# Optimization experiments

Hardware: AMD Instinct MI355X
Metric: run time of the kernel (lower is better)

## Reference

```python
import jax, jax.numpy as jnp
import numpy as np

B, T, H = 256, 48, 512   # batch, timesteps, hidden (= size_seq feature dim)
S = H                    # size_seq == hidden feature dim (dim_seq_in = S+1)
K = 4                    # k_wk_ahead


def setup_inputs() -> dict:
    key = jax.random.key(0)
    ks = jax.random.split(key, 20)
    g = lambda k, shp: (jax.random.normal(k, shp, dtype=jnp.float32) * 0.05)
    inp = {
        "hiddens": jax.random.normal(ks[0], (B, T, S), dtype=jnp.float32),
        "allys": jax.random.normal(ks[1], (B, T), dtype=jnp.float32),
        "k_wk_ahead": K,
        # InputAttention params (Linear stored as [in, out])
        "Wh": g(ks[2], (H, S)), "bh": g(ks[3], (S,)),
        "Ws": g(ks[4], (S, S)), "bs": g(ks[5], (S,)),
        "Wo": g(ks[6], (S, 1)), "bo": g(ks[7], (1,)),
        # GRU params (torch layout: [3H, in]/[3H, H], gates ordered r,z,n)
        "W_ih": g(ks[8], (3 * H, S + 1)), "W_hh": g(ks[9], (3 * H, H)),
        "b_ih": g(ks[10], (3 * H,)), "b_hh": g(ks[11], (3 * H,)),
        # out_layer MLP: H->H/2->H/4->H/8->1 with LeakyReLU after each
        "W1": g(ks[12], (H, H // 2)), "b1": g(ks[13], (H // 2,)),
        "W2": g(ks[14], (H // 2, H // 4)), "b2": g(ks[15], (H // 4,)),
        "W3": g(ks[16], (H // 4, H // 8)), "b3": g(ks[17], (H // 8,)),
        "W4": g(ks[18], (H // 8, 1)), "b4": g(ks[19], (1,)),
    }
    return inp


def _gru_step(x, h, W_ih, W_hh, b_ih, b_hh):
    # torch GRU cell: gates ordered (reset, update, new)
    gi = x @ W_ih.T + b_ih          # [B, 3H]
    gh = h @ W_hh.T + b_hh          # [B, 3H]
    ir, iz, inn = jnp.split(gi, 3, axis=-1)
    hr, hz, hn = jnp.split(gh, 3, axis=-1)
    r = jax.nn.sigmoid(ir + hr)
    z = jax.nn.sigmoid(iz + hz)
    n = jnp.tanh(inn + r * hn)
    return (1.0 - z) * n + z * h


def reference(hiddens, allys, k_wk_ahead, Wh, bh, Ws, bs, Wo, bo,
              W_ih, W_hh, b_ih, b_hh, W1, b1, W2, b2, W3, b3, W4, b4):
    Bb, Tt, Ss = hiddens.shape
    # linearSignals(hiddens) is time-step-invariant: precompute once
    ls = hiddens @ Ws + bs                      # [B, T, S]

    def step(d_prev, ally_t):
        lh = d_prev @ Wh + bh                   # [B, S]
        e = jnp.tanh(lh[:, None, :] + ls) @ Wo + bo    # [B, T, 1]
        att = jax.nn.softmax(e, axis=1)[..., 0]        # [B, T]
        c = jnp.einsum('bt,bts->bs', att, hiddens)     # [B, S]
        x = jnp.concatenate([c, ally_t[:, None]], axis=1)   # [B, S+1]
        d = _gru_step(x, d_prev, W_ih, W_hh, b_ih, b_hh)
        return d, c

    d0 = jnp.zeros((Bb, W_hh.shape[1]), dtype=hiddens.dtype)
    d_last, cs = jax.lax.scan(step, d0, jnp.swapaxes(allys, 0, 1))
    c_last = cs[-1]                             # c_vectors[:, -1]

    def mlp(d):
        h = jax.nn.leaky_relu(d @ W1 + b1)
        h = jax.nn.leaky_relu(h @ W2 + b2)
        h = jax.nn.leaky_relu(h @ W3 + b3)
        return jax.nn.leaky_relu(h @ W4 + b4)   # dropout is identity in eval

    outs = []
    last_d = d_last
    for _ in range(k_wk_ahead):
        out = mlp(last_d)                       # [B, 1]
        outs.append(out)
        x = jnp.concatenate([c_last, out], axis=1)
        last_d = _gru_step(x, last_d, W_ih, W_hh, b_ih, b_hh)
    return jnp.stack(outs, axis=1)[..., 0]      # [B, K]
```

## Files before the change

kernel.cpp:

```cpp
#include <hip/hip_runtime.h>
#include <cstdio>

#ifndef __has_builtin
#define __has_builtin(x) 0
#endif

#define NB      256
#define NT      48
#define NS      512
#define KAHEAD  4
#define NTHREADS 1024
#define NBLOCKS  256
#define GSIZE    32

#define RSTRIDE  528
#define XSLOT    524
#define NKS      33

#define WS_D     0
#define WS_X     135168
#define WS_LH    270336
#define WS_BAR   401408
#define WS_WAH   401664
#define WS_WAL   942336
#define WS_WIH   1483008
#define WS_WIL   1888512
#define WS_FLOATS 2294016

#define L_XHI    0
#define L_XLO    34048
#define L_LSB    68096
#define L_GH     117248
#define L_GI     123776
#define L_LH     130304
#define L_WO     132352
#define L_E      134400
#define L_ATT    134656
#define L_CP     134912
#define L_H1P    136960
#define L_H1S    141056
#define L_H2P    142080
#define L_H2S    144128
#define L_H3P    144640
#define LDS_BYTES 145664

#define XROWB    1064

typedef float  f4v __attribute__((ext_vector_type(4)));
typedef short  s4v __attribute__((ext_vector_type(4)));
typedef unsigned short u4v __attribute__((ext_vector_type(4)));

#if __has_builtin(__builtin_amdgcn_mfma_f32_16x16x16bf16_1k)
__device__ __forceinline__ f4v MFMA16(s4v a, s4v b, f4v c) {
    return __builtin_amdgcn_mfma_f32_16x16x16bf16_1k(a, b, c, 0, 0, 0);
}
#else
typedef short s8v __attribute__((ext_vector_type(8)));
__device__ __forceinline__ f4v MFMA16(s4v a, s4v b, f4v c) {
    s8v A = { a[0], a[1], a[2], a[3], 0, 0, 0, 0 };
    s8v B = { b[0], b[1], b[2], b[3], 0, 0, 0, 0 };
    return __builtin_amdgcn_mfma_f32_16x16x32_bf16(A, B, c, 0, 0, 0);
}
#endif

__device__ __forceinline__ float frcp_(float x) {
#if __has_builtin(__builtin_amdgcn_rcpf)
    return __builtin_amdgcn_rcpf(x);
#else
    return 1.0f / x;
#endif
}
__device__ __forceinline__ float ftanh_(float x) {
    float e = __expf(2.0f * x);
    return 1.0f - 2.0f * frcp_(e + 1.0f);
}
__device__ __forceinline__ float fsig_(float x) { return frcp_(1.0f + __expf(-x)); }
__device__ __forceinline__ float lrelu_(float x) { return fmaxf(x, 0.01f * x); }
__device__ __forceinline__ unsigned short rne16_(unsigned u) {
    return (unsigned short)((u + 0x7FFFu + ((u >> 16) & 1u)) >> 16);
}
__device__ __forceinline__ float bf2f_(unsigned short b) {
    return __uint_as_float(((unsigned)b) << 16);
}
__host__ __device__ __forceinline__ void split2_(float v, unsigned short& hi, unsigned short& lo) {
    unsigned u = __float_as_uint(v);
    unsigned short h = (unsigned short)((u + 0x7FFFu + ((u >> 16) & 1u)) >> 16);
    float hf = __uint_as_float(((unsigned)h) << 16);
    float lof = v - hf;
    unsigned ul = __float_as_uint(lof);
    hi = h;
    lo = (unsigned short)((ul + 0x7FFFu + ((ul >> 16) & 1u)) >> 16);
}

__device__ __forceinline__ void cstore1(float* p, float v) {
    asm volatile("global_store_dword %0, %1, off sc1" :: "v"(p), "v"(v) : "memory");
}
__device__ __forceinline__ f4v cload4(const float* p) {
    f4v v;
    asm volatile("global_load_dwordx4 %0, %1, off sc1" : "=v"(v) : "v"(p));
    return v;
}
__device__ __forceinline__ float cload1(const float* p) {
    float v;
    asm volatile("global_load_dword %0, %1, off sc1" : "=v"(v) : "v"(p));
    return v;
}
__device__ __forceinline__ void cwait() {
    asm volatile("s_waitcnt vmcnt(0)" ::: "memory");
    __builtin_amdgcn_sched_barrier(0);
}

__device__ __forceinline__ void gbar(unsigned* bar, unsigned* epoch) {
    asm volatile("s_waitcnt vmcnt(0)" ::: "memory");
    __syncthreads();
    if (threadIdx.x == 0) {
        *epoch += GSIZE;
        __hip_atomic_fetch_add(bar, 1u, __ATOMIC_RELAXED, __HIP_MEMORY_SCOPE_AGENT);
        unsigned target = *epoch;
        int guard = 0;
        while (__hip_atomic_load(bar, __ATOMIC_RELAXED, __HIP_MEMORY_SCOPE_AGENT) < target) {
#if __has_builtin(__builtin_amdgcn_s_sleep)
            __builtin_amdgcn_s_sleep(2);
#endif
            if (++guard > (1 << 22)) break;
        }
    }
    __syncthreads();
}

__device__ __forceinline__ void cvtStore_(char* hiB, char* loB, int idx, f4v v) {
    unsigned row = (unsigned)idx / 528u;
    unsigned col = (unsigned)idx - row * 528u;
    u4v h, l;
    #pragma unroll
    for (int i = 0; i < 4; ++i) {
        unsigned short hh, ll;
        split2_(v[i], hh, ll);
        h[i] = hh; l[i] = ll;
    }
    *(u4v*)(hiB + row * XROWB + col * 2) = h;
    *(u4v*)(loB + row * XROWB + col * 2) = l;
}

__device__ __forceinline__ void stagePanel(const float* __restrict__ gsrc,
                                           char* __restrict__ hiB,
                                           char* __restrict__ loB, int tid) {
    f4v v0 = cload4(gsrc + tid * 4);
    f4v v1 = cload4(gsrc + 4096 + tid * 4);
    f4v v2 = cload4(gsrc + 8192 + tid * 4);
    f4v v3 = cload4(gsrc + 12288 + tid * 4);
    f4v v4 = {0.f, 0.f, 0.f, 0.f};
    if (tid < 128) v4 = cload4(gsrc + 16384 + tid * 4);
    cwait();
    cvtStore_(hiB, loB, tid * 4, v0);
    cvtStore_(hiB, loB, 4096 + tid * 4, v1);
    cvtStore_(hiB, loB, 8192 + tid * 4, v2);
    cvtStore_(hiB, loB, 12288 + tid * 4, v3);
    if (tid < 128) cvtStore_(hiB, loB, 16384 + tid * 4, v4);
}

__device__ __forceinline__ void gemmA(const char* smem, const unsigned short* BH,
        const unsigned short* BL, int cix, int g, int tid, float* ghs,
        float* lhw, const float* bh, const float* bhh, bool doLH) {
    const int w = tid >> 6;
    if (w >= 8) return;
    const int l = tid & 63, mt = w & 1, nt = w >> 1;
    const char* A  = smem + L_XHI + (mt * 16 + (l & 15)) * XROWB + ((l >> 4) << 3);
    const char* Al = A + (L_XLO - L_XHI);
    const int bbase = ((cix * 4 + nt) * NKS) * 256 + (l << 2);
    f4v acc = {0.f, 0.f, 0.f, 0.f};
    #pragma unroll 3
    for (int ks = 0; ks < NKS; ++ks) {
        s4v ah = *(const s4v*)(A + ks * 32);
        s4v al = *(const s4v*)(Al + ks * 32);
        s4v bhv = *(const s4v*)(BH + bbase + ks * 256);
        s4v blv = *(const s4v*)(BL + bbase + ks * 256);
        acc = MFMA16(ah, bhv, acc);
        acc = MFMA16(al, bhv, acc);
        acc = MFMA16(ah, blv, acc);
    }
    const int jgl = cix * 16 + (l & 15);
    const int rowL = mt * 16 + ((l >> 4) << 2);
    if (nt == 0) {
        if (doLH) {
            float b = bh[jgl];
            #pragma unroll
            for (int r = 0; r < 4; ++r)
                cstore1(lhw + (long)(g * 32 + rowL + r) * NS + jgl, acc[r] + b);
        }
    } else {
        float b = bhh[(nt - 1) * 512 + jgl];
        #pragma unroll
        for (int r = 0; r < 4; ++r)
            ghs[(nt - 1) * 544 + (rowL + r) * 17 + (l & 15)] = acc[r] + b;
    }
}

__device__ __forceinline__ void gemmC(const char* smem, const unsigned short* BH,
        const unsigned short* BL, int cix, int tid, float* gis, const float* bih) {
    const int w = tid >> 6;
    if (w >= 6) return;
    const int l = tid & 63, mt = w & 1, nt = w >> 1;
    const char* A  = smem + L_XHI + (mt * 16 + (l & 15)) * XROWB + ((l >> 4) << 3);
    const char* Al = A + (L_XLO - L_XHI);
    const int bbase = ((cix * 3 + nt) * NKS) * 256 + (l << 2);
    f4v acc = {0.f, 0.f, 0.f, 0.f};
    #pragma unroll 3
    for (int ks = 0; ks < NKS; ++ks) {
        s4v ah = *(const s4v*)(A + ks * 32);
        s4v al = *(const s4v*)(Al + ks * 32);
        s4v bhv = *(const s4v*)(BH + bbase + ks * 256);
        s4v blv = *(const s4v*)(BL + bbase + ks * 256);
        acc = MFMA16(ah, bhv, acc);
        acc = MFMA16(al, bhv, acc);
        acc = MFMA16(ah, blv, acc);
    }
    const int jgl = cix * 16 + (l & 15);
    const int rowL = mt * 16 + ((l >> 4) << 2);
    float b = bih[nt * 512 + jgl];
    #pragma unroll
    for (int r = 0; r < 4; ++r)
        gis[nt * 544 + (rowL + r) * 17 + (l & 15)] = acc[r] + b;
}

__global__ void prep_kernel(const float* __restrict__ Whh,
                            const float* __restrict__ Wih,
                            const float* __restrict__ Wh,
                            float* __restrict__ ws) {
    long i = (long)blockIdx.x * blockDim.x + threadIdx.x;
    long stride = (long)gridDim.x * blockDim.x;
    unsigned short* waH = (unsigned short*)(ws + WS_WAH);
    unsigned short* waL = (unsigned short*)(ws + WS_WAL);
    unsigned short* wiH = (unsigned short*)(ws + WS_WIH);
    unsigned short* wiL = (unsigned short*)(ws + WS_WIL);

    for (long p = i; p < 270336; p += stride) {
        int l = (int)(p & 63);
        int t = (int)(p >> 6);
        int ks = t % NKS, u = t / NKS;
        int nt = u & 3, cix = u >> 2;
        int jg = cix * 16 + (l & 15);
        #pragma unroll
        for (int e = 0; e < 4; ++e) {
            int pc = ks * 16 + ((l >> 4) << 2) + e;
            int kq = pc / 132, ko = pc - kq * 132;
            float wv = 0.f;
            if (ko < 128) {
                int k = kq * 128 + ko;
                wv = (nt == 0) ? Wh[(long)k * 512 + jg]
                               : Whh[((long)((nt - 1) * 512 + jg)) * 512 + k];
            }
            unsigned short hh, ll;
            split2_(wv, hh, ll);
            waH[p * 4 + e] = hh; waL[p * 4 + e] = ll;
        }
    }
    for (long p = i; p < 202752; p += stride) {
        int l = (int)(p & 63);
        int t = (int)(p >> 6);
        int ks = t % NKS, u = t / NKS;
        int nt = u % 3, cix = u / 3;
        int jg = cix * 16 + (l & 15);
        #pragma unroll
        for (int e = 0; e < 4; ++e) {
            int pc = ks * 16 + ((l >> 4) << 2) + e;
            int kq = pc / 132, ko = pc - kq * 132;
            float wv = 0.f;
            int k = -1;
            if (ko < 128) k = kq * 128 + ko;
            else if (pc == XSLOT) k = 512;
            if (k >= 0) wv = Wih[((long)(nt * 512 + jg)) * 513 + k];
            unsigned short hh, ll;
            split2_(wv, hh, ll);
            wiH[p * 4 + e] = hh; wiL[p * 4 + e] = ll;
        }
    }
    for (long p = i; p < 270336; p += stride) ws[WS_D + p] = 0.0f;
    if (i < 256) ((unsigned*)(ws + WS_BAR))[i] = 0u;
}

__global__ void __launch_bounds__(NTHREADS, 4) fused_kernel(
        const float* __restrict__ hiddens, const float* __restrict__ allys,
        const float* __restrict__ Ws, const float* __restrict__ bs,
        const float* __restrict__ Wo, const float* __restrict__ bo,
        const float* __restrict__ bh,
        const float* __restrict__ b_ih, const float* __restrict__ b_hh,
        const float* __restrict__ W1, const float* __restrict__ b1,
        const float* __restrict__ W2, const float* __restrict__ b2,
        const float* __restrict__ W3, const float* __restrict__ b3,
        const float* __restrict__ W4, const float* __restrict__ b4,
        float* __restrict__ ws, float* __restrict__ out) {
    const int tid = threadIdx.x;
    const int bid = blockIdx.x;
    const int g = bid >> 5, cix = bid & 31, myb = bid;

    float* dw  = ws + WS_D;
    float* xw  = ws + WS_X;
    float* lhw = ws + WS_LH;
    const unsigned short* waH = (const unsigned short*)(ws + WS_WAH);
    const unsigned short* waL = (const unsigned short*)(ws + WS_WAL);
    const unsigned short* wiH = (const unsigned short*)(ws + WS_WIH);
    const unsigned short* wiL = (const unsigned short*)(ws + WS_WIL);
    unsigned* bar = (unsigned*)(ws + WS_BAR) + (g << 5);
    unsigned epoch = 0;

    extern __shared__ char smem[];
    char*           xhi   = smem + L_XHI;
    char*           xlo   = smem + L_XLO;
    unsigned short* lsb   = (unsigned short*)(smem + L_LSB);
    float*          ghs   = (float*)(smem + L_GH);
    float*          gis   = (float*)(smem + L_GI);
    float*          lh_s  = (float*)(smem + L_LH);
    float*          wo_s  = (float*)(smem + L_WO);
    float*          e_s   = (float*)(smem + L_E);
    float*          att_s = (float*)(smem + L_ATT);
    float*          cp_s  = (float*)(smem + L_CP);
    float*          h1p   = (float*)(smem + L_H1P);
    float*          h1s   = (float*)(smem + L_H1S);
    float*          h2p   = (float*)(smem + L_H2P);
    float*          h2s   = (float*)(smem + L_H2S);
    float*          h3p   = (float*)(smem + L_H3P);

    const int sS = tid & 511, th = tid >> 9;
    const int rowE = tid >> 4, jE = tid & 15;
    const int jgE = cix * 16 + jE;
    const int jmapE = ((jgE >> 7) * 132) + (jgE & 127);
    const float* gPanelD = dw + (long)g * GSIZE * RSTRIDE;
    const float* gPanelX = xw + (long)g * GSIZE * RSTRIDE;

    float hreg[24];

    if (tid < NS) wo_s[tid] = Wo[tid];

    {
        float* scratch = (float*)(smem + L_XHI);
        for (int ch = 0; ch < 2; ++ch) {
            __syncthreads();
            {
                const float* src = hiddens + ((long)myb * NT + ch * 24) * NS;
                int idx = tid * 12;
                const f4v* s4 = (const f4v*)(src + idx);
                f4v* d4 = (f4v*)(scratch + idx);
                d4[0] = s4[0]; d4[1] = s4[1]; d4[2] = s4[2];
            }
            __syncthreads();
            if (th == ch) {
                #pragma unroll
                for (int q = 0; q < 24; ++q) hreg[q] = scratch[q * 512 + sS];
            }
            {
                const int tl = th * 12;
                float acc[12];
                #pragma unroll
                for (int q = 0; q < 12; ++q) acc[q] = 0.0f;
                for (int k = 0; k < NS; k += 4) {
                    float w0 = Ws[(k + 0) * NS + sS];
                    float w1 = Ws[(k + 1) * NS + sS];
                    float w2 = Ws[(k + 2) * NS + sS];
                    float w3 = Ws[(k + 3) * NS + sS];
                    #pragma unroll
                    for (int q = 0; q < 12; ++q) {
                        f4v h4 = *(const f4v*)(scratch + (tl + q) * 512 + k);
                        acc[q] = fmaf(h4.x, w0, fmaf(h4.y, w1, fmaf(h4.z, w2, fmaf(h4.w, w3, acc[q]))));
                    }
                }
                float bsv = bs[sS];
                #pragma unroll
                for (int q = 0; q < 12; ++q)
                    lsb[(ch * 24 + tl + q) * NS + sS] = rne16_(__float_as_uint(acc[q] + bsv));
            }
        }
    }
    __syncthreads();

    const float bo0 = bo[0];

    for (int t = 0; t < NT; ++t) {
        stagePanel(gPanelD, xhi, xlo, tid);
        __syncthreads();
        gemmA(smem, waH, waL, cix, g, tid, ghs, lhw, bh, b_hh, true);
        gbar(bar, &epoch);

        if (tid < 128) {
            f4v v = cload4(lhw + (long)myb * NS + tid * 4);
            cwait();
            *(f4v*)(lh_s + tid * 4) = v;
        }
        if (tid == 0) cstore1(xw + (long)myb * RSTRIDE + XSLOT, allys[myb * NT + t]);
        __syncthreads();
        {
            const int wv = tid >> 6, ln = tid & 63;
            for (int q = 0; q < 3; ++q) {
                const int tt = wv * 3 + q;
                float p = 0.f;
                #pragma unroll
                for (int i2 = 0; i2 < 8; ++i2) {
                    int s = ln + (i2 << 6);
                    p = fmaf(wo_s[s], ftanh_(lh_s[s] + bf2f_(lsb[tt * NS + s])), p);
                }
                #pragma unroll
                for (int off = 32; off >= 1; off >>= 1) p += __shfl_xor(p, off, 64);
                if (ln == 0) e_s[tt] = p + bo0;
            }
        }
        __syncthreads();
        if (tid < 64) {
            float v = (tid < NT) ? e_s[tid] : -1e30f;
            float m = v;
            #pragma unroll
            for (int off = 32; off >= 1; off >>= 1) m = fmaxf(m, __shfl_xor(m, off, 64));
            float ex = (tid < NT) ? __expf(v - m) : 0.0f;
            float ssum = ex;
            #pragma unroll
            for (int off = 32; off >= 1; off >>= 1) ssum += __shfl_xor(ssum, off, 64);
            if (tid < NT) att_s[tid] = ex * frcp_(ssum);
        }
        __syncthreads();
        {
            float p = 0.f;
            #pragma unroll
            for (int q = 0; q < 24; ++q) p = fmaf(att_s[th * 24 + q], hreg[q], p);
            if (th == 0) cp_s[sS] = p;
            __syncthreads();
            if (th == 1)
                cstore1(xw + (long)myb * RSTRIDE + ((sS >> 7) * 132) + (sS & 127), p + cp_s[sS]);
        }
        gbar(bar, &epoch);

        float hp = 0.f;
        if (tid < 512) hp = cload1(dw + (long)(g * 32 + rowE) * RSTRIDE + jmapE);
        stagePanel(gPanelX, xhi, xlo, tid);
        __syncthreads();
        gemmC(smem, wiH, wiL, cix, tid, gis, b_ih);
        __syncthreads();
        cwait();
        if (tid < 512) {
            float gr = gis[rowE * 17 + jE]        + ghs[rowE * 17 + jE];
            float gz = gis[544 + rowE * 17 + jE]  + ghs[544 + rowE * 17 + jE];
            float gni = gis[1088 + rowE * 17 + jE];
            float gnh = ghs[1088 + rowE * 17 + jE];
            float rg = fsig_(gr);
            float zg = fsig_(gz);
            float ng = ftanh_(gni + rg * gnh);
            cstore1(dw + (long)(g * 32 + rowE) * RSTRIDE + jmapE, (1.f - zg) * ng + zg * hp);
        }
        gbar(bar, &epoch);
    }

    for (int kk = 0; kk < KAHEAD; ++kk) {
        {
            float v = 0.f;
            if (tid < NS) v = cload1(dw + (long)myb * RSTRIDE + ((tid >> 7) * 132) + (tid & 127));
            cwait();
            if (tid < NS) lh_s[tid] = v;
        }
        __syncthreads();
        {
            int n = tid & 255, q4 = tid >> 8;
            const float* av = lh_s + q4 * 128;
            const float* wp = W1 + (long)(q4 * 128) * 256 + n;
            float acc = 0.f;
            #pragma unroll 4
            for (int k2 = 0; k2 < 128; ++k2) { acc = fmaf(av[k2], wp[0], acc); wp += 256; }
            h1p[n * 4 + q4] = acc;
        }
        __syncthreads();
        if (tid < 256) {
            float v = h1p[tid * 4] + h1p[tid * 4 + 1] + h1p[tid * 4 + 2] + h1p[tid * 4 + 3];
            h1s[tid] = lrelu_(v + b1[tid]);
        }
        __syncthreads();
        if (tid < 512) {
            int n = tid & 127, q4 = tid >> 7;
            const float* av = h1s + q4 * 64;
            const float* wp = W2 + (long)(q4 * 64) * 128 + n;
            float acc = 0.f;
            #pragma unroll 4
            for (int k2 = 0; k2 < 64; ++k2) { acc = fmaf(av[k2], wp[0], acc); wp += 128; }
            h2p[n * 4 + q4] = acc;
        }
        __syncthreads();
        if (tid < 128) {
            float v = h2p[tid * 4] + h2p[tid * 4 + 1] + h2p[tid * 4 + 2] + h2p[tid * 4 + 3];
            h2s[tid] = lrelu_(v + b2[tid]);
        }
        __syncthreads();
        if (tid < 256) {
            int n = tid & 63, q4 = tid >> 6;
            const float* av = h2s + q4 * 32;
            const float* wp = W3 + (long)(q4 * 32) * 64 + n;
            float acc = 0.f;
            #pragma unroll 4
            for (int k2 = 0; k2 < 32; ++k2) { acc = fmaf(av[k2], wp[0], acc); wp += 64; }
            h3p[n * 4 + q4] = acc;
        }
        __syncthreads();
        if (tid < 64) {
            float v = h3p[tid * 4] + h3p[tid * 4 + 1] + h3p[tid * 4 + 2] + h3p[tid * 4 + 3];
            float h3v = lrelu_(v + b3[tid]);
            float p = h3v * W4[tid];
            #pragma unroll
            for (int off = 32; off >= 1; off >>= 1) p += __shfl_xor(p, off, 64);
            if (tid == 0) {
                float o = lrelu_(p + b4[0]);
                out[myb * KAHEAD + kk] = o;
                cstore1(xw + (long)myb * RSTRIDE + XSLOT, o);
            }
        }
        if (kk < KAHEAD - 1) {
            gbar(bar, &epoch);
            float hp = 0.f;
            if (tid < 512) hp = cload1(dw + (long)(g * 32 + rowE) * RSTRIDE + jmapE);
            stagePanel(gPanelD, xhi, xlo, tid);
            __syncthreads();
            gemmA(smem, waH, waL, cix, g, tid, ghs, lhw, bh, b_hh, false);
            __syncthreads();
            stagePanel(gPanelX, xhi, xlo, tid);
            __syncthreads();
            gemmC(smem, wiH, wiL, cix, tid, gis, b_ih);
            __syncthreads();
            cwait();
            if (tid < 512) {
                float gr = gis[rowE * 17 + jE]        + ghs[rowE * 17 + jE];
                float gz = gis[544 + rowE * 17 + jE]  + ghs[544 + rowE * 17 + jE];
                float gni = gis[1088 + rowE * 17 + jE];
                float gnh = ghs[1088 + rowE * 17 + jE];
                float rg = fsig_(gr);
                float zg = fsig_(gz);
                float ng = ftanh_(gni + rg * gnh);
                cstore1(dw + (long)(g * 32 + rowE) * RSTRIDE + jmapE, (1.f - zg) * ng + zg * hp);
            }
            gbar(bar, &epoch);
        }
    }
}

extern "C" void kernel_launch(void* const* d_in, const int* in_sizes, int n_in,
                              void* d_out, int out_size, void* d_ws, size_t ws_size,
                              hipStream_t stream) {
    const float* hiddens = (const float*)d_in[0];
    const float* allys   = (const float*)d_in[1];
    const float* Wh   = (const float*)d_in[3];
    const float* bh   = (const float*)d_in[4];
    const float* Ws   = (const float*)d_in[5];
    const float* bs   = (const float*)d_in[6];
    const float* Wo   = (const float*)d_in[7];
    const float* bo   = (const float*)d_in[8];
    const float* W_ih = (const float*)d_in[9];
    const float* W_hh = (const float*)d_in[10];
    const float* b_ih = (const float*)d_in[11];
    const float* b_hh = (const float*)d_in[12];
    const float* W1 = (const float*)d_in[13];
    const float* b1 = (const float*)d_in[14];
    const float* W2 = (const float*)d_in[15];
    const float* b2 = (const float*)d_in[16];
    const float* W3 = (const float*)d_in[17];
    const float* b3 = (const float*)d_in[18];
    const float* W4 = (const float*)d_in[19];
    const float* b4 = (const float*)d_in[20];
    float* wsf = (float*)d_ws;
    float* outf = (float*)d_out;

    if (ws_size < (size_t)WS_FLOATS * sizeof(float)) {
        fprintf(stderr, "kernel_launch: workspace too small (%zu < %zu)\n",
                ws_size, (size_t)WS_FLOATS * sizeof(float));
        return;
    }

    prep_kernel<<<dim3(2048), dim3(256), 0, stream>>>(W_hh, W_ih, Wh, wsf);

    (void)hipFuncSetAttribute((const void*)fused_kernel,
                              hipFuncAttributeMaxDynamicSharedMemorySize, LDS_BYTES);

    void* args[] = { &hiddens, &allys, &Ws, &bs, &Wo, &bo, &bh,
                     &b_ih, &b_hh, &W1, &b1, &W2, &b2, &W3, &b3, &W4, &b4,
                     &wsf, &outf };
    hipError_t e = hipLaunchCooperativeKernel((void*)fused_kernel,
                                              dim3(NBLOCKS), dim3(NTHREADS),
                                              args, LDS_BYTES, stream);
    if (e != hipSuccess) {
        fprintf(stderr, "coop launch failed (%d); plain fallback\n", (int)e);
        (void)hipGetLastError();
        fused_kernel<<<dim3(NBLOCKS), dim3(NTHREADS), LDS_BYTES, stream>>>(
            hiddens, allys, Ws, bs, Wo, bo, bh, b_ih, b_hh,
            W1, b1, W2, b2, W3, b3, W4, b4, wsf, outf);
    }
}
```

Baseline: 2.100 ms.

## Use 32x32 MFMA for GRU gemms, MFMA ls precompute, XCC-local block groups

Replaces the per-step 16x16 MFMA GEMMs (8 and 6 waves) with 32x32x16 bf16 MFMA on 2 waves, repacking weights in prep. The fp32 scalar Ws projection of hiddens becomes a split-bf16 MFMA GEMM with prepacked Ws, and hidden registers load straight from global. Blocks pick their group and column index from the hardware XCC id with an atomic rank so each 32-block barrier group stays on one XCC, and the coherence bits drop from sc1 to sc0. It also pads the LDS row stride and drops a redundant wait. The risks are that fewer waves in the GEMMs lengthen the serial critical path, and that sc0 plus XCC grouping assumes exactly 32 resident blocks per XCC for correctness.

```diff
diff --git a/kernel.cpp b/kernel.cpp
--- a/kernel.cpp
+++ b/kernel.cpp
@@ -12,10 +12,10 @@
 #define NTHREADS 1024
 #define NBLOCKS  256
 #define GSIZE    32
-
 #define RSTRIDE  528
 #define XSLOT    524
 #define NKS      33
+#define XROWB    1120
 
 #define WS_D     0
 #define WS_X     135168
@@ -23,39 +23,44 @@
 #define WS_BAR   401408
 #define WS_WAH   401664
 #define WS_WAL   942336
-#define WS_WIH   1483008
-#define WS_WIL   1888512
-#define WS_FLOATS 2294016
+#define WS_WCH   1483008
+#define WS_WCL   2023680
+#define WS_WSH   2564352
+#define WS_WSL   2695424
+#define WS_FLOATS 2826496
 
 #define L_XHI    0
-#define L_XLO    34048
-#define L_LSB    68096
-#define L_GH     117248
-#define L_GI     123776
-#define L_LH     130304
-#define L_WO     132352
-#define L_E      134400
-#define L_ATT    134656
-#define L_CP     134912
-#define L_H1P    136960
-#define L_H1S    141056
-#define L_H2P    142080
-#define L_H2S    144128
-#define L_H3P    144640
-#define LDS_BYTES 145664
-
-#define XROWB    1064
-
-typedef float  f4v __attribute__((ext_vector_type(4)));
-typedef short  s4v __attribute__((ext_vector_type(4)));
+#define L_XLO    35840
+#define L_LSB    71680
+#define L_GH     120832
+#define L_GI     127360
+#define L_LH     133888
+#define L_WO     135936
+#define L_E      137984
+#define L_ATT    138240
+#define L_CP     138496
+#define L_H1P    140544
+#define L_H1S    144640
+#define L_H2P    145664
+#define L_H2S    147712
+#define L_H3P    148224
+#define L_MISC   149248
+#define LDS_BYTES 149264
+
+typedef float  f4v  __attribute__((ext_vector_type(4)));
+typedef float  f16v __attribute__((ext_vector_type(16)));
+typedef short  s4v  __attribute__((ext_vector_type(4)));
+typedef short  s8v  __attribute__((ext_vector_type(8)));
 typedef unsigned short u4v __attribute__((ext_vector_type(4)));
 
+__device__ __forceinline__ f16v MFMA32(s8v a, s8v b, f16v c) {
+    return __builtin_amdgcn_mfma_f32_32x32x16_bf16(a, b, c, 0, 0, 0);
+}
 #if __has_builtin(__builtin_amdgcn_mfma_f32_16x16x16bf16_1k)
 __device__ __forceinline__ f4v MFMA16(s4v a, s4v b, f4v c) {
     return __builtin_amdgcn_mfma_f32_16x16x16bf16_1k(a, b, c, 0, 0, 0);
 }
 #else
-typedef short s8v __attribute__((ext_vector_type(8)));
 __device__ __forceinline__ f4v MFMA16(s4v a, s4v b, f4v c) {
     s8v A = { a[0], a[1], a[2], a[3], 0, 0, 0, 0 };
     s8v B = { b[0], b[1], b[2], b[3], 0, 0, 0, 0 };
@@ -86,23 +91,22 @@
     unsigned u = __float_as_uint(v);
     unsigned short h = (unsigned short)((u + 0x7FFFu + ((u >> 16) & 1u)) >> 16);
     float hf = __uint_as_float(((unsigned)h) << 16);
-    float lof = v - hf;
-    unsigned ul = __float_as_uint(lof);
+    unsigned ul = __float_as_uint(v - hf);
     hi = h;
     lo = (unsigned short)((ul + 0x7FFFu + ((ul >> 16) & 1u)) >> 16);
 }
 
 __device__ __forceinline__ void cstore1(float* p, float v) {
-    asm volatile("global_store_dword %0, %1, off sc1" :: "v"(p), "v"(v) : "memory");
+    asm volatile("global_store_dword %0, %1, off sc0" :: "v"(p), "v"(v) : "memory");
 }
 __device__ __forceinline__ f4v cload4(const float* p) {
     f4v v;
-    asm volatile("global_load_dwordx4 %0, %1, off sc1" : "=v"(v) : "v"(p));
+    asm volatile("global_load_dwordx4 %0, %1, off sc0" : "=v"(v) : "v"(p));
     return v;
 }
 __device__ __forceinline__ float cload1(const float* p) {
     float v;
-    asm volatile("global_load_dword %0, %1, off sc1" : "=v"(v) : "v"(p));
+    asm volatile("global_load_dword %0, %1, off sc0" : "=v"(v) : "v"(p));
     return v;
 }
 __device__ __forceinline__ void cwait() {
@@ -133,15 +137,10 @@
     unsigned col = (unsigned)idx - row * 528u;
     u4v h, l;
     #pragma unroll
-    for (int i = 0; i < 4; ++i) {
-        unsigned short hh, ll;
-        split2_(v[i], hh, ll);
-        h[i] = hh; l[i] = ll;
-    }
+    for (int i = 0; i < 4; ++i) { unsigned short hh, ll; split2_(v[i], hh, ll); h[i] = hh; l[i] = ll; }
     *(u4v*)(hiB + row * XROWB + col * 2) = h;
     *(u4v*)(loB + row * XROWB + col * 2) = l;
 }
-
 __device__ __forceinline__ void stagePanel(const float* __restrict__ gsrc,
                                            char* __restrict__ hiB,
                                            char* __restrict__ loB, int tid) {
@@ -159,120 +158,192 @@
     if (tid < 128) cvtStore_(hiB, loB, 16384 + tid * 4, v4);
 }
 
-__device__ __forceinline__ void gemmA(const char* smem, const unsigned short* BH,
-        const unsigned short* BL, int cix, int g, int tid, float* ghs,
-        float* lhw, const float* bh, const float* bhh, bool doLH) {
+__device__ __forceinline__ void gemmA32(const char* smem, const unsigned short* BH,
+        const unsigned short* BL, int cix, int g, int tid, float* ghs, float* lhw,
+        const float* bh, const float* bhh, bool doLH) {
     const int w = tid >> 6;
-    if (w >= 8) return;
-    const int l = tid & 63, mt = w & 1, nt = w >> 1;
+    if (w >= 2) return;
+    const int l = tid & 63;
+    const char* A  = smem + L_XHI + (l & 31) * XROWB + ((l >> 5) << 4);
+    const char* Al = smem + L_XLO + (l & 31) * XROWB + ((l >> 5) << 4);
+    const unsigned short* ph = BH + ((long)(cix * 2 + w) * NKS) * 512 + (l << 3);
+    const unsigned short* pl = BL + ((long)(cix * 2 + w) * NKS) * 512 + (l << 3);
+    f16v acc = {0,0,0,0,0,0,0,0,0,0,0,0,0,0,0,0};
+    #pragma unroll 4
+    for (int ks = 0; ks < NKS; ++ks) {
+        s8v ah = *(const s8v*)(A + ks * 32);
+        s8v al = *(const s8v*)(Al + ks * 32);
+        s8v bh8 = *(const s8v*)(ph + ks * 512);
+        s8v bl8 = *(const s8v*)(pl + ks * 512);
+        acc = MFMA32(ah, bh8, acc);
+        acc = MFMA32(al, bh8, acc);
+        acc = MFMA32(ah, bl8, acc);
+    }
+    const int c = w * 32 + (l & 31);
+    const int rb = (l >> 5) << 2;
+    if (c < 16) {
+        if (doLH) {
+            const int j = cix * 16 + c;
+            const float b = bh[j];
+            #pragma unroll
+            for (int r = 0; r < 16; ++r) {
+                int row = (r & 3) + ((r >> 2) << 3) + rb;
+                cstore1(lhw + (long)(g * 32 + row) * NS + j, acc[r] + b);
+            }
+        }
+    } else {
+        const int gate = (c - 16) >> 4, jj = (c - 16) & 15;
+        const float b = bhh[gate * 512 + cix * 16 + jj];
+        #pragma unroll
+        for (int r = 0; r < 16; ++r) {
+            int row = (r & 3) + ((r >> 2) << 3) + rb;
+            ghs[gate * 544 + row * 17 + jj] = acc[r] + b;
+        }
+    }
+}
+
+__device__ __forceinline__ void gemmC32(const char* smem, const unsigned short* BH,
+        const unsigned short* BL, int cix, int tid, float* gis, const float* bih) {
+    const int w = tid >> 6;
+    if (w >= 2) return;
+    const int l = tid & 63;
+    const char* A  = smem + L_XHI + (l & 31) * XROWB + ((l >> 5) << 4);
+    const char* Al = smem + L_XLO + (l & 31) * XROWB + ((l >> 5) << 4);
+    const unsigned short* ph = BH + ((long)(cix * 2 + w) * NKS) * 512 + (l << 3);
+    const unsigned short* pl = BL + ((long)(cix * 2 + w) * NKS) * 512 + (l << 3);
+    f16v acc = {0,0,0,0,0,0,0,0,0,0,0,0,0,0,0,0};
+    #pragma unroll 4
+    for (int ks = 0; ks < NKS; ++ks) {
+        s8v ah = *(const s8v*)(A + ks * 32);
+        s8v al = *(const s8v*)(Al + ks * 32);
+        s8v bh8 = *(const s8v*)(ph + ks * 512);
+        s8v bl8 = *(const s8v*)(pl + ks * 512);
+        acc = MFMA32(ah, bh8, acc);
+        acc = MFMA32(al, bh8, acc);
+        acc = MFMA32(ah, bl8, acc);
+    }
+    const int c = w * 32 + (l & 63 & 31);
+    const int rb = (l >> 5) << 2;
+    if (c < 48) {
+        const int gate = c >> 4, jj = c & 15;
+        const float b = bih[gate * 512 + cix * 16 + jj];
+        #pragma unroll
+        for (int r = 0; r < 16; ++r) {
+            int row = (r & 3) + ((r >> 2) << 3) + rb;
+            gis[gate * 544 + row * 17 + jj] = acc[r] + b;
+        }
+    }
+}
+
+__device__ __forceinline__ void lsGemm(const char* smem, const unsigned short* WH,
+        const unsigned short* WL, int tid, int ch, unsigned short* lsb, const float* bs) {
+    const int w = tid >> 6, l = tid & 63;
+    const int mt = w & 1, ng = w >> 1;
     const char* A  = smem + L_XHI + (mt * 16 + (l & 15)) * XROWB + ((l >> 4) << 3);
-    const char* Al = A + (L_XLO - L_XHI);
-    const int bbase = ((cix * 4 + nt) * NKS) * 256 + (l << 2);
-    f4v acc = {0.f, 0.f, 0.f, 0.f};
-    #pragma unroll 3
-    for (int ks = 0; ks < NKS; ++ks) {
+    const char* Al = smem + L_XLO + (mt * 16 + (l & 15)) * XROWB + ((l >> 4) << 3);
+    f4v acc[4] = {{0,0,0,0},{0,0,0,0},{0,0,0,0},{0,0,0,0}};
+    for (int ks = 0; ks < 32; ++ks) {
         s4v ah = *(const s4v*)(A + ks * 32);
         s4v al = *(const s4v*)(Al + ks * 32);
-        s4v bhv = *(const s4v*)(BH + bbase + ks * 256);
-        s4v blv = *(const s4v*)(BL + bbase + ks * 256);
-        acc = MFMA16(ah, bhv, acc);
-        acc = MFMA16(al, bhv, acc);
-        acc = MFMA16(ah, blv, acc);
-    }
-    const int jgl = cix * 16 + (l & 15);
-    const int rowL = mt * 16 + ((l >> 4) << 2);
-    if (nt == 0) {
-        if (doLH) {
-            float b = bh[jgl];
-            #pragma unroll
-            for (int r = 0; r < 4; ++r)
-                cstore1(lhw + (long)(g * 32 + rowL + r) * NS + jgl, acc[r] + b);
-        }
-    } else {
-        float b = bhh[(nt - 1) * 512 + jgl];
         #pragma unroll
-        for (int r = 0; r < 4; ++r)
-            ghs[(nt - 1) * 544 + (rowL + r) * 17 + (l & 15)] = acc[r] + b;
-    }
-}
-
-__device__ __forceinline__ void gemmC(const char* smem, const unsigned short* BH,
-        const unsigned short* BL, int cix, int tid, float* gis, const float* bih) {
-    const int w = tid >> 6;
-    if (w >= 6) return;
-    const int l = tid & 63, mt = w & 1, nt = w >> 1;
-    const char* A  = smem + L_XHI + (mt * 16 + (l & 15)) * XROWB + ((l >> 4) << 3);
-    const char* Al = A + (L_XLO - L_XHI);
-    const int bbase = ((cix * 3 + nt) * NKS) * 256 + (l << 2);
-    f4v acc = {0.f, 0.f, 0.f, 0.f};
-    #pragma unroll 3
-    for (int ks = 0; ks < NKS; ++ks) {
-        s4v ah = *(const s4v*)(A + ks * 32);
-        s4v al = *(const s4v*)(Al + ks * 32);
-        s4v bhv = *(const s4v*)(BH + bbase + ks * 256);
-        s4v blv = *(const s4v*)(BL + bbase + ks * 256);
-        acc = MFMA16(ah, bhv, acc);
-        acc = MFMA16(al, bhv, acc);
-        acc = MFMA16(ah, blv, acc);
-    }
-    const int jgl = cix * 16 + (l & 15);
-    const int rowL = mt * 16 + ((l >> 4) << 2);
-    float b = bih[nt * 512 + jgl];
+        for (int i = 0; i < 4; ++i) {
+            const unsigned short* bp  = WH + (((ng * 4 + i) * 32 + ks) << 8) + (l << 2);
+            const unsigned short* blp = WL + (((ng * 4 + i) * 32 + ks) << 8) + (l << 2);
+            s4v bh = *(const s4v*)bp;
+            s4v bl = *(const s4v*)blp;
+            acc[i] = MFMA16(ah, bh, acc[i]);
+            acc[i] = MFMA16(al, bh, acc[i]);
+            acc[i] = MFMA16(ah, bl, acc[i]);
+        }
+    }
+    const int rb = mt * 16 + ((l >> 4) << 2);
     #pragma unroll
-    for (int r = 0; r < 4; ++r)
-        gis[nt * 544 + (rowL + r) * 17 + (l & 15)] = acc[r] + b;
+    for (int i = 0; i < 4; ++i) {
+        const int n = (ng * 4 + i) * 16 + (l & 15);
+        const float bsv = bs[n];
+        #pragma unroll
+        for (int r = 0; r < 4; ++r) {
+            int row = rb + r;
+            if (row < 24)
+                lsb[(ch * 24 + row) * NS + n] = rne16_(__float_as_uint(acc[i][r] + bsv));
+        }
+    }
 }
 
 __global__ void prep_kernel(const float* __restrict__ Whh,
                             const float* __restrict__ Wih,
                             const float* __restrict__ Wh,
+                            const float* __restrict__ Ws,
                             float* __restrict__ ws) {
     long i = (long)blockIdx.x * blockDim.x + threadIdx.x;
     long stride = (long)gridDim.x * blockDim.x;
     unsigned short* waH = (unsigned short*)(ws + WS_WAH);
     unsigned short* waL = (unsigned short*)(ws + WS_WAL);
-    unsigned short* wiH = (unsigned short*)(ws + WS_WIH);
-    unsigned short* wiL = (unsigned short*)(ws + WS_WIL);
-
-    for (long p = i; p < 270336; p += stride) {
+    unsigned short* wcH = (unsigned short*)(ws + WS_WCH);
+    unsigned short* wcL = (unsigned short*)(ws + WS_WCL);
+    unsigned short* wsH = (unsigned short*)(ws + WS_WSH);
+    unsigned short* wsL = (unsigned short*)(ws + WS_WSL);
+
+    for (long p = i; p < 135168; p += stride) {
         int l = (int)(p & 63);
-        int t = (int)(p >> 6);
-        int ks = t % NKS, u = t / NKS;
-        int nt = u & 3, cix = u >> 2;
-        int jg = cix * 16 + (l & 15);
+        long t = p >> 6;
+        int ks = (int)(t % 33);
+        int u  = (int)(t / 33);
+        int half = u & 1, cix = u >> 1;
+        int c = half * 32 + (l & 31);
         #pragma unroll
-        for (int e = 0; e < 4; ++e) {
-            int pc = ks * 16 + ((l >> 4) << 2) + e;
+        for (int e = 0; e < 8; ++e) {
+            int pc = ks * 16 + ((l >> 5) << 3) + e;
             int kq = pc / 132, ko = pc - kq * 132;
             float wv = 0.f;
             if (ko < 128) {
                 int k = kq * 128 + ko;
-                wv = (nt == 0) ? Wh[(long)k * 512 + jg]
-                               : Whh[((long)((nt - 1) * 512 + jg)) * 512 + k];
+                if (c < 16) wv = Wh[(long)k * 512 + cix * 16 + c];
+                else {
+                    int gate = (c - 16) >> 4, j = cix * 16 + ((c - 16) & 15);
+                    wv = Whh[((long)(gate * 512 + j)) * 512 + k];
+                }
             }
-            unsigned short hh, ll;
-            split2_(wv, hh, ll);
-            waH[p * 4 + e] = hh; waL[p * 4 + e] = ll;
-        }
-    }
-    for (long p = i; p < 202752; p += stride) {
+            unsigned short hh, ll; split2_(wv, hh, ll);
+            waH[p * 8 + e] = hh; waL[p * 8 + e] = ll;
+        }
+    }
+    for (long p = i; p < 135168; p += stride) {
         int l = (int)(p & 63);
-        int t = (int)(p >> 6);
-        int ks = t % NKS, u = t / NKS;
-        int nt = u % 3, cix = u / 3;
-        int jg = cix * 16 + (l & 15);
+        long t = p >> 6;
+        int ks = (int)(t % 33);
+        int u  = (int)(t / 33);
+        int half = u & 1, cix = u >> 1;
+        int c = half * 32 + (l & 31);
+        #pragma unroll
+        for (int e = 0; e < 8; ++e) {
+            int pc = ks * 16 + ((l >> 5) << 3) + e;
+            int kq = pc / 132, ko = pc - kq * 132;
+            float wv = 0.f;
+            if (c < 48) {
+                int k = -1;
+                if (ko < 128) k = kq * 128 + ko;
+                else if (pc == XSLOT) k = 512;
+                if (k >= 0) {
+                    int gate = c >> 4, j = cix * 16 + (c & 15);
+                    wv = Wih[((long)(gate * 512 + j)) * 513 + k];
+                }
+            }
+            unsigned short hh, ll; split2_(wv, hh, ll);
+            wcH[p * 8 + e] = hh; wcL[p * 8 + e] = ll;
+        }
+    }
+    for (long p = i; p < 65536; p += stride) {
+        int l = (int)(p & 63);
+        long t = p >> 6;
+        int ks = (int)(t & 31), nt = (int)(t >> 5);
+        int n = nt * 16 + (l & 15);
         #pragma unroll
         for (int e = 0; e < 4; ++e) {
-            int pc = ks * 16 + ((l >> 4) << 2) + e;
-            int kq = pc / 132, ko = pc - kq * 132;
-            float wv = 0.f;
-            int k = -1;
-            if (ko < 128) k = kq * 128 + ko;
-            else if (pc == XSLOT) k = 512;
-            if (k >= 0) wv = Wih[((long)(nt * 512 + jg)) * 513 + k];
-            unsigned short hh, ll;
-            split2_(wv, hh, ll);
-            wiH[p * 4 + e] = hh; wiL[p * 4 + e] = ll;
+            int k = ks * 16 + ((l >> 4) << 2) + e;
+            float wv = Ws[(long)k * 512 + n];
+            unsigned short hh, ll; split2_(wv, hh, ll);
+            wsH[p * 4 + e] = hh; wsL[p * 4 + e] = ll;
         }
     }
     for (long p = i; p < 270336; p += stride) ws[WS_D + p] = 0.0f;
@@ -281,7 +352,7 @@
 
 __global__ void __launch_bounds__(NTHREADS, 4) fused_kernel(
         const float* __restrict__ hiddens, const float* __restrict__ allys,
-        const float* __restrict__ Ws, const float* __restrict__ bs,
+        const float* __restrict__ bs,
         const float* __restrict__ Wo, const float* __restrict__ bo,
         const float* __restrict__ bh,
         const float* __restrict__ b_ih, const float* __restrict__ b_hh,
@@ -291,18 +362,17 @@
         const float* __restrict__ W4, const float* __restrict__ b4,
         float* __restrict__ ws, float* __restrict__ out) {
     const int tid = threadIdx.x;
-    const int bid = blockIdx.x;
-    const int g = bid >> 5, cix = bid & 31, myb = bid;
 
     float* dw  = ws + WS_D;
     float* xw  = ws + WS_X;
     float* lhw = ws + WS_LH;
     const unsigned short* waH = (const unsigned short*)(ws + WS_WAH);
     const unsigned short* waL = (const unsigned short*)(ws + WS_WAL);
-    const unsigned short* wiH = (const unsigned short*)(ws + WS_WIH);
-    const unsigned short* wiL = (const unsigned short*)(ws + WS_WIL);
-    unsigned* bar = (unsigned*)(ws + WS_BAR) + (g << 5);
-    unsigned epoch = 0;
+    const unsigned short* wcH = (const unsigned short*)(ws + WS_WCH);
+    const unsigned short* wcL = (const unsigned short*)(ws + WS_WCL);
+    const unsigned short* wsH = (const unsigned short*)(ws + WS_WSH);
+    const unsigned short* wsL = (const unsigned short*)(ws + WS_WSL);
+    unsigned* barbase = (unsigned*)(ws + WS_BAR);
 
     extern __shared__ char smem[];
     char*           xhi   = smem + L_XHI;
@@ -320,6 +390,22 @@
     float*          h2p   = (float*)(smem + L_H2P);
     float*          h2s   = (float*)(smem + L_H2S);
     float*          h3p   = (float*)(smem + L_H3P);
+    int*            misc  = (int*)(smem + L_MISC);
+
+    if (tid == 0) {
+        unsigned xcc;
+        asm volatile("s_getreg_b32 %0, hwreg(HW_REG_XCC_ID)" : "=s"(xcc));
+        int gx = (int)(xcc & 7u);
+        unsigned rk = __hip_atomic_fetch_add(barbase + gx * 32 + 1, 1u,
+                                             __ATOMIC_RELAXED, __HIP_MEMORY_SCOPE_AGENT);
+        misc[0] = gx;
+        misc[1] = (int)(rk & 31u);
+    }
+    __syncthreads();
+    const int g = misc[0], cix = misc[1];
+    const int myb = g * 32 + cix;
+    unsigned* bar = barbase + (g << 5);
+    unsigned epoch = 0;
 
     const int sS = tid & 511, th = tid >> 9;
     const int rowE = tid >> 4, jE = tid & 15;
@@ -329,47 +415,30 @@
     const float* gPanelX = xw + (long)g * GSIZE * RSTRIDE;
 
     float hreg[24];
-
     if (tid < NS) wo_s[tid] = Wo[tid];
-
-    {
-        float* scratch = (float*)(smem + L_XHI);
-        for (int ch = 0; ch < 2; ++ch) {
-            __syncthreads();
-            {
-                const float* src = hiddens + ((long)myb * NT + ch * 24) * NS;
-                int idx = tid * 12;
-                const f4v* s4 = (const f4v*)(src + idx);
-                f4v* d4 = (f4v*)(scratch + idx);
-                d4[0] = s4[0]; d4[1] = s4[1]; d4[2] = s4[2];
+    #pragma unroll
+    for (int q = 0; q < 24; ++q)
+        hreg[q] = hiddens[((long)myb * NT + th * 24 + q) * NS + sS];
+
+    for (int ch = 0; ch < 2; ++ch) {
+        __syncthreads();
+        {
+            const float* src = hiddens + ((long)myb * NT + ch * 24) * NS;
+            const int i0 = tid * 12;
+            #pragma unroll
+            for (int j3 = 0; j3 < 3; ++j3) {
+                f4v v = *(const f4v*)(src + i0 + j3 * 4);
+                int idx = i0 + j3 * 4;
+                int row = idx >> 9, col = idx & 511;
+                u4v h, l;
+                #pragma unroll
+                for (int e = 0; e < 4; ++e) { unsigned short hh, ll; split2_(v[e], hh, ll); h[e] = hh; l[e] = ll; }
+                *(u4v*)(xhi + row * XROWB + col * 2) = h;
+                *(u4v*)(xlo + row * XROWB + col * 2) = l;
             }
-            __syncthreads();
-            if (th == ch) {
-                #pragma unroll
-                for (int q = 0; q < 24; ++q) hreg[q] = scratch[q * 512 + sS];
-            }
-            {
-                const int tl = th * 12;
-                float acc[12];
-                #pragma unroll
-                for (int q = 0; q < 12; ++q) acc[q] = 0.0f;
-                for (int k = 0; k < NS; k += 4) {
-                    float w0 = Ws[(k + 0) * NS + sS];
-                    float w1 = Ws[(k + 1) * NS + sS];
-                    float w2 = Ws[(k + 2) * NS + sS];
-                    float w3 = Ws[(k + 3) * NS + sS];
-                    #pragma unroll
-                    for (int q = 0; q < 12; ++q) {
-                        f4v h4 = *(const f4v*)(scratch + (tl + q) * 512 + k);
-                        acc[q] = fmaf(h4.x, w0, fmaf(h4.y, w1, fmaf(h4.z, w2, fmaf(h4.w, w3, acc[q]))));
-                    }
-                }
-                float bsv = bs[sS];
-                #pragma unroll
-                for (int q = 0; q < 12; ++q)
-                    lsb[(ch * 24 + tl + q) * NS + sS] = rne16_(__float_as_uint(acc[q] + bsv));
-            }
-        }
+        }
+        __syncthreads();
+        lsGemm(smem, wsH, wsL, tid, ch, lsb, bs);
     }
     __syncthreads();
 
@@ -378,7 +447,7 @@
     for (int t = 0; t < NT; ++t) {
         stagePanel(gPanelD, xhi, xlo, tid);
         __syncthreads();
-        gemmA(smem, waH, waL, cix, g, tid, ghs, lhw, bh, b_hh, true);
+        gemmA32(smem, waH, waL, cix, g, tid, ghs, lhw, bh, b_hh, true);
         gbar(bar, &epoch);
 
         if (tid < 128) {
@@ -431,12 +500,11 @@
         if (tid < 512) hp = cload1(dw + (long)(g * 32 + rowE) * RSTRIDE + jmapE);
         stagePanel(gPanelX, xhi, xlo, tid);
         __syncthreads();
-        gemmC(smem, wiH, wiL, cix, tid, gis, b_ih);
-        __syncthreads();
-        cwait();
+        gemmC32(smem, wcH, wcL, cix, tid, gis, b_ih);
+        __syncthreads();
         if (tid < 512) {
-            float gr = gis[rowE * 17 + jE]        + ghs[rowE * 17 + jE];
-            float gz = gis[544 + rowE * 17 + jE]  + ghs[544 + rowE * 17 + jE];
+            float gr  = gis[rowE * 17 + jE]        + ghs[rowE * 17 + jE];
+            float gz  = gis[544 + rowE * 17 + jE]  + ghs[544 + rowE * 17 + jE];
             float gni = gis[1088 + rowE * 17 + jE];
             float gnh = ghs[1088 + rowE * 17 + jE];
             float rg = fsig_(gr);
@@ -513,16 +581,15 @@
             if (tid < 512) hp = cload1(dw + (long)(g * 32 + rowE) * RSTRIDE + jmapE);
             stagePanel(gPanelD, xhi, xlo, tid);
             __syncthreads();
-            gemmA(smem, waH, waL, cix, g, tid, ghs, lhw, bh, b_hh, false);
+            gemmA32(smem, waH, waL, cix, g, tid, ghs, lhw, bh, b_hh, false);
             __syncthreads();
             stagePanel(gPanelX, xhi, xlo, tid);
             __syncthreads();
-            gemmC(smem, wiH, wiL, cix, tid, gis, b_ih);
+            gemmC32(smem, wcH, wcL, cix, tid, gis, b_ih);
             __syncthreads();
-            cwait();
             if (tid < 512) {
-                float gr = gis[rowE * 17 + jE]        + ghs[rowE * 17 + jE];
-                float gz = gis[544 + rowE * 17 + jE]  + ghs[544 + rowE * 17 + jE];
+                float gr  = gis[rowE * 17 + jE]        + ghs[rowE * 17 + jE];
+                float gz  = gis[544 + rowE * 17 + jE]  + ghs[544 + rowE * 17 + jE];
                 float gni = gis[1088 + rowE * 17 + jE];
                 float gnh = ghs[1088 + rowE * 17 + jE];
                 float rg = fsig_(gr);
@@ -567,12 +634,12 @@
         return;
     }
 
-    prep_kernel<<<dim3(2048), dim3(256), 0, stream>>>(W_hh, W_ih, Wh, wsf);
+    prep_kernel<<<dim3(2048), dim3(256), 0, stream>>>(W_hh, W_ih, Wh, Ws, wsf);
 
     (void)hipFuncSetAttribute((const void*)fused_kernel,
                               hipFuncAttributeMaxDynamicSharedMemorySize, LDS_BYTES);
 
-    void* args[] = { &hiddens, &allys, &Ws, &bs, &Wo, &bo, &bh,
+    void* args[] = { &hiddens, &allys, &bs, &Wo, &bo, &bh,
                      &b_ih, &b_hh, &W1, &b1, &W2, &b2, &W3, &b3, &W4, &b4,
                      &wsf, &outf };
     hipError_t e = hipLaunchCooperativeKernel((void*)fused_kernel,
@@ -582,7 +649,7 @@
         fprintf(stderr, "coop launch failed (%d); plain fallback\n", (int)e);
         (void)hipGetLastError();
         fused_kernel<<<dim3(NBLOCKS), dim3(NTHREADS), LDS_BYTES, stream>>>(
-            hiddens, allys, Ws, bs, Wo, bo, bh, b_ih, b_hh,
+            hiddens, allys, bs, Wo, bo, bh, b_ih, b_hh,
             W1, b1, W2, b2, W3, b3, W4, b4, wsf, outf);
     }
 }
```

Result: slower. 4.641 ms (+121.0%).
